# Optimization experiments

Measured on AMD Instinct MI355X. Metric: run time of the kernel, lower is better.

## Reference

```python
import jax, jax.numpy as jnp
from jax import lax
import numpy as np

NF = 64      # feature channels
G = 8        # mask groups
NBR = 3      # top-k neighbors
PATCH = 7    # correlation patch size (patches[0])
CORK = 3     # correlation / unfold kernel size
PAD_COR = 1  # (CORK-1)//2
PAD_S = 4    # PAD_COR + (PATCH-1)//2
ADD = 6      # 2*PAD_S - CORK + 1
B, H, W = 4, 96, 96


def leaky(x):
    return jnp.where(x >= 0, x, 0.1 * x)


def _conv(x, w, b, pad):
    y = lax.conv_general_dilated(x, w, (1, 1), [(pad[0], pad[0]), (pad[1], pad[1])],
                                 dimension_numbers=('NCHW', 'OIHW', 'NCHW'))
    return y + b[None, :, None, None]


def _normalize(x, eps=1e-12):
    n = jnp.sqrt(jnp.sum(x * x, axis=1, keepdims=True))
    return x / jnp.maximum(n, eps)


def _correlation(f1, f2):
    # spatial-correlation-sampler: kernel=3, patch=7, stride=1, pad=1, dilations=1
    # out[b, ph*7+pw, i, j] = sum_{c,u,v} f1p[b,c,i+u,j+v] * f2p[b,c,i+u+ph-3, j+v+pw-3]
    # (unnormalized; only topk indices are consumed downstream, so any positive
    #  constant scale is irrelevant)
    Bx, C, Hx, Wx = f1.shape
    f1p = jnp.pad(f1, ((0, 0), (0, 0), (PAD_COR, PAD_COR), (PAD_COR, PAD_COR)))
    f2p = jnp.pad(f2, ((0, 0), (0, 0), (PAD_S, PAD_S), (PAD_S, PAD_S)))
    outs = []
    for ph in range(PATCH):
        for pw in range(PATCH):
            s = jnp.sum(f1p * f2p[:, :, ph:ph + Hx + 2, pw:pw + Wx + 2], axis=1)  # [B,H+2,W+2]
            o = sum(s[:, u:u + Hx, v:v + Wx] for u in range(CORK) for v in range(CORK))
            outs.append(o)
    return jnp.stack(outs, axis=1)  # [B, 49, H, W]


def setup_inputs() -> dict:
    key = jax.random.key(0)
    ks = jax.random.split(key, 16)

    def wt(k, shape):
        fan_in = shape[1] * shape[2] * shape[3]
        return jax.random.normal(k, shape, jnp.float32) * (1.0 / np.sqrt(fan_in))

    return {
        'ref_fea_l': jax.random.normal(ks[0], (B, NF, H, W), jnp.float32),
        'w1': wt(ks[1], (NF, NF * 2, 3, 3)), 'b1': jnp.zeros((NF,), jnp.float32),
        'w2': wt(ks[2], (NF, NF, 3, 3)),     'b2': jnp.zeros((NF,), jnp.float32),
        'w3': wt(ks[3], (NF, NF, 7, 1)),     'b3': jnp.zeros((NF,), jnp.float32),
        'w4': wt(ks[4], (NF, NF, 1, 7)),     'b4': jnp.zeros((NF,), jnp.float32),
        'wm': wt(ks[5], (G * CORK ** 2, NF, 3, 3)), 'bm': jnp.zeros((G * CORK ** 2,), jnp.float32),
        'wnn': wt(ks[6], (NF, NF * NBR, 3, 3)), 'bnn': jnp.zeros((NF,), jnp.float32),
        'wf': wt(ks[7], (NF, NF * 2, 3, 3)),    'bf': jnp.zeros((NF,), jnp.float32),
    }


def reference(ref_fea_l, w1, b1, w2, b2, w3, b3, w4, b4, wm, bm, wnn, bnn, wf, bf):
    Bx, C, Hx, Wx = ref_fea_l.shape
    nbr_fea = ref_fea_l  # aliased in the original forward

    # mask branch
    x = jnp.concatenate([nbr_fea, ref_fea_l], axis=1)
    x = leaky(_conv(x, w1, b1, (1, 1)))
    x = leaky(_conv(x, w2, b2, (1, 1)))
    x = leaky(_conv(x, w3, b3, (3, 0)))
    x = leaky(_conv(x, w4, b4, (0, 3)))
    mask = _conv(x, wm, bm, (1, 1)).reshape(Bx, G, 1, CORK ** 2, Hx, Wx)

    # correlation + topk neighbor displacements
    nref = _normalize(ref_fea_l)
    corr = _correlation(nref, nref)                     # [B,49,H,W]
    _, idx = lax.top_k(corr.transpose(0, 2, 3, 1), NBR)  # [B,H,W,NBR]

    # flat indices into the (H+6)x(W+6) unfold grid
    ph = idx // PATCH
    pw = idx % PATCH
    yy = jnp.arange(Hx)[:, None, None]
    xx = jnp.arange(Wx)[None, :, None]
    flat = ((ph + yy) * (Wx + ADD) + (pw + xx)).reshape(Bx, Hx * Wx * NBR)

    # unfold (im2col) of nbr features with pad 4, then gather chosen 3x3 patches
    nbr_pad = jnp.pad(nbr_fea, ((0, 0), (0, 0), (PAD_S, PAD_S), (PAD_S, PAD_S)))
    patches = lax.conv_general_dilated_patches(nbr_pad, (CORK, CORK), (1, 1), 'VALID',
                                               dimension_numbers=('NCHW', 'OIHW', 'NCHW'))
    pl = patches.reshape(Bx, C * CORK ** 2, -1).transpose(0, 2, 1)  # [B, (H+6)(W+6), C*9]
    gath = jnp.take_along_axis(pl, flat[:, :, None], axis=1)        # [B, HW*NBR, C*9]
    gath = gath.reshape(Bx * Hx * Wx, NBR * C, CORK, CORK)

    # conv over gathered patches then modulated mask-weighted reduce
    g = leaky(_conv(gath, wnn, bnn, (1, 1)))                         # [BHW, C, 3, 3]
    g = g.reshape(Bx, Hx, Wx, C, CORK ** 2).transpose(0, 3, 4, 1, 2)
    g = g.reshape(Bx, G, C // G, CORK ** 2, Hx, Wx)
    agg = leaky(jnp.sum(g * mask, axis=3).reshape(Bx, C, Hx, Wx))

    out = leaky(_conv(jnp.concatenate([ref_fea_l, agg], axis=1), wf, bf, (1, 1)))
    return out
```

## Files before the change

kernel.cpp:

```cpp
#include <hip/hip_runtime.h>
#include <hip/hip_bf16.h>

constexpr int BATCH = 4;
constexpr int H = 96, W = 96, HW = H * W;
constexpr int NBR = 3;

using bf16x8 = __attribute__((ext_vector_type(8))) short;
using f32x4 = __attribute__((ext_vector_type(4))) float;

static __device__ __forceinline__ float leakyf(float x) {
    return x >= 0.f ? x : 0.1f * x;
}

static __device__ __forceinline__ short f2bf(float x) {
    __hip_bfloat16 h = __float2bfloat16(x);
    return *reinterpret_cast<short*>(&h);
}

static __device__ __forceinline__ float bf2f(short s) {
    __hip_bfloat16 h = *reinterpret_cast<__hip_bfloat16*>(&s);
    return __bfloat162float(h);
}

__global__ __launch_bounds__(256) void k_pre(const float* __restrict__ ref,
                                             short* __restrict__ reft,
                                             float* __restrict__ nrn) {
    int p = blockIdx.x * 256 + threadIdx.x;
    if (p >= BATCH * HW) return;
    int b = p / HW, ij = p % HW;
    const float* src = ref + b * 64 * HW + ij;
    float v[64];
    float ss = 0.f;
#pragma unroll
    for (int c = 0; c < 64; ++c) {
        v[c] = src[c * HW];
        ss += v[c] * v[c];
    }
    float inv = 1.f / fmaxf(sqrtf(ss), 1e-12f);
    short* rd = reft + (size_t)p * 64;
#pragma unroll
    for (int cc = 0; cc < 8; ++cc) {
        bf16x8 o;
#pragma unroll
        for (int j = 0; j < 8; ++j) o[j] = f2bf(v[cc * 8 + j]);
        *(bf16x8*)(rd + cc * 8) = o;
    }
    float* nd = nrn + b * 64 * HW + ij;
#pragma unroll
    for (int c = 0; c < 64; ++c) nd[c * HW] = v[c] * inv;
}

static __device__ __forceinline__ void packw(const float* __restrict__ src,
                                             short* __restrict__ dst, int i,
                                             int OC, int ICt, int ICsrc, int KH,
                                             int KW, int NT, int fold) {
    int e = i & 7, l = (i >> 3) & 63;
    int rest = i >> 9;
    int nt = rest % NT;
    rest /= NT;
    int ICK = ICt >> 5;
    int kk = rest % ICK;
    int tap = rest / ICK;
    int ic = kk * 32 + (l >> 4) * 8 + e;
    int oc = nt * 16 + (l & 15);
    int u = tap / KW, v = tap % KW;
    float val = 0.f;
    if (oc < OC) {
        val = src[((oc * ICsrc + ic) * KH + u) * KW + v];
        if (fold) val += src[((oc * ICsrc + 64 + ic) * KH + u) * KW + v];
    }
    dst[i] = f2bf(val);
}

constexpr int E1 = 36864, E2 = 36864, E3 = 28672, E4 = 28672, E5 = 46080,
              E6 = 73728, E7 = 110592;
constexpr int C1 = E1, C2 = C1 + E2, C3 = C2 + E3, C4 = C3 + E4, C5 = C4 + E5,
              C6 = C5 + E6, C7 = C6 + E7, CT = C7 + 8;
__global__ void k_prep_all(const float* __restrict__ w1,
                           const float* __restrict__ w2,
                           const float* __restrict__ w3,
                           const float* __restrict__ w4,
                           const float* __restrict__ wm,
                           const float* __restrict__ wf,
                           const float* __restrict__ wnn,
                           short* __restrict__ P1, short* __restrict__ P2,
                           short* __restrict__ P3, short* __restrict__ P4,
                           short* __restrict__ PM, short* __restrict__ PF,
                           short* __restrict__ B2, short* __restrict__ zpad) {
    int i = blockIdx.x * 256 + threadIdx.x;
    if (i >= CT) return;
    if (i < C1) {
        packw(w1, P1, i, 64, 64, 128, 3, 3, 4, 1);
    } else if (i < C2) {
        packw(w2, P2, i - C1, 64, 64, 64, 3, 3, 4, 0);
    } else if (i < C3) {
        packw(w3, P3, i - C2, 64, 64, 64, 7, 1, 4, 0);
    } else if (i < C4) {
        packw(w4, P4, i - C3, 64, 64, 64, 1, 7, 4, 0);
    } else if (i < C5) {
        packw(wm, PM, i - C4, 72, 64, 64, 3, 3, 5, 0);
    } else if (i < C6) {
        packw(wf, PF, i - C5, 64, 128, 128, 3, 3, 4, 0);
    } else if (i < C7) {
        int j = i - C6;
        int e = j & 7, l = (j >> 3) & 63;
        int t = (j >> 9) % 9;
        int h2 = (j / (512 * 9)) % 2;
        int n = (j / (512 * 9 * 2)) % 3;
        int nt = j / (512 * 9 * 2 * 3);
        int oc = nt * 16 + (l & 15);
        int c = h2 * 32 + (l >> 4) * 8 + e;
        int u = t / 3, v = t % 3;
        B2[j] = f2bf(wnn[((oc * 192 + n * 64 + c) * 3 + u) * 3 + v]);
    } else {
        zpad[i - C7] = 0;
    }
}

template <int KH, int KW, int IC, int OC, int OMODE, bool BLDS, int NSPL>
__global__ __launch_bounds__(256) void k_cmfma(
    const short* __restrict__ inA, const short* __restrict__ inB,
    const short* __restrict__ Bp, const float* __restrict__ bias,
    void* __restrict__ outp) {
    constexpr int TI = 8, TJ = 16;
    constexpr int PH = (KH - 1) / 2, PW = (KW - 1) / 2;
    constexpr int LR = TI + KH - 1, LC = TJ + KW - 1;
    constexpr int ICB = IC * 2;
    constexpr int LS = (ICB == 128) ? 7 : 8;
    constexpr int ICK = IC / 32;
    constexpr int NTF = (OC + 15) / 16;
    constexpr int NTb = NTF / NSPL;
    constexpr int TAPS = KH * KW;
    constexpr int NOCT = ICB / 16;
    __shared__ char Xs[LR * LC * ICB];
    __shared__ short Bs[BLDS ? TAPS * ICK * NTb * 512 : 8];
    const int tj0 = blockIdx.x * TJ, ti0 = blockIdx.y * TI;
    const int b = blockIdx.z / NSPL;
    const int nt0 = (blockIdx.z % NSPL) * NTb;
    const int tid = threadIdx.x;
    if (BLDS) {
        for (int u2 = tid; u2 < TAPS * ICK * NTb * 64; u2 += 256) {
            int l2 = u2 & 63;
            int rest = u2 >> 6;
            int nt = rest % NTb;
            int qk = rest / NTb;
            ((bf16x8*)Bs)[u2] = ((const bf16x8*)Bp)[(qk * NTF + nt0 + nt) * 64 + l2];
        }
    }
    for (int u2 = tid; u2 < LR * LC * NOCT; u2 += 256) {
        int oct = u2 % NOCT;
        int hp = u2 / NOCT;
        int hr = hp / LC, hc = hp % LC;
        int gi = ti0 + hr - PH, gj = tj0 + hc - PW;
        bf16x8 v = {};
        if (gi >= 0 && gi < H && gj >= 0 && gj < W) {
            const short* s = (oct < 8) ? inA : inB;
            v = *(const bf16x8*)(s + (size_t)(b * HW + gi * W + gj) * 64 +
                                 (oct & 7) * 8);
        }
        int byte = hp * ICB + oct * 16;
        byte ^= ((byte >> LS) & 7) << 4;
        *(bf16x8*)(Xs + byte) = v;
    }
    __syncthreads();
    const int wave = tid >> 6, l = tid & 63;
    const int r = l & 15, q = l >> 4;
    const int mt0 = wave * 2;
    int p0 = mt0 * 16 + r, p1 = p0 + 16;
    int li0 = p0 >> 4, lj0 = p0 & 15, li1 = p1 >> 4, lj1 = p1 & 15;
    f32x4 acc[2][NTb] = {};
#pragma unroll
    for (int t = 0; t < TAPS; ++t) {
        const int u = t / KW, v = t % KW;
        int hp0 = (li0 + u) * LC + (lj0 + v);
        int hp1 = (li1 + u) * LC + (lj1 + v);
#pragma unroll
        for (int kk = 0; kk < ICK; ++kk) {
            int ab0 = hp0 * ICB + kk * 64 + q * 16;
            ab0 ^= ((ab0 >> LS) & 7) << 4;
            int ab1 = hp1 * ICB + kk * 64 + q * 16;
            ab1 ^= ((ab1 >> LS) & 7) << 4;
            bf16x8 a0 = *(const bf16x8*)(Xs + ab0);
            bf16x8 a1 = *(const bf16x8*)(Xs + ab1);
            const short* bbase =
                BLDS ? (const short*)Bs + (t * ICK + kk) * NTb * 512 + l * 8
                     : Bp + ((t * ICK + kk) * NTF + nt0) * 512 + l * 8;
#pragma unroll
            for (int nt = 0; nt < NTb; ++nt) {
                bf16x8 bv = *(const bf16x8*)(bbase + nt * 512);
                acc[0][nt] =
                    __builtin_amdgcn_mfma_f32_16x16x32_bf16(a0, bv, acc[0][nt], 0, 0, 0);
                acc[1][nt] =
                    __builtin_amdgcn_mfma_f32_16x16x32_bf16(a1, bv, acc[1][nt], 0, 0, 0);
            }
        }
    }
    const int col = l & 15;
#pragma unroll
    for (int mt = 0; mt < 2; ++mt)
#pragma unroll
        for (int nt = 0; nt < NTb; ++nt) {
            int oc = (nt0 + nt) * 16 + col;
            float bs = (oc < OC) ? bias[oc] : 0.f;
#pragma unroll
            for (int j = 0; j < 4; ++j) {
                int p = (mt0 + mt) * 16 + q * 4 + j;
                int gi = ti0 + (p >> 4), gj = tj0 + (p & 15);
                float val = acc[mt][nt][j] + bs;
                if (OMODE == 0) {
                    val = leakyf(val);
                    *((short*)outp + (size_t)(b * HW + gi * W + gj) * 64 + oc) =
                        f2bf(val);
                } else if (OMODE == 1) {
                    if (oc < 72)
                        *((short*)outp + (size_t)(b * HW + gi * W + gj) * 72 + oc) =
                            f2bf(val);
                } else {
                    val = leakyf(val);
                    *((float*)outp + (size_t)(b * 64 + oc) * HW + gi * W + gj) = val;
                }
            }
        }
}

__global__ void k_corr2(const float* __restrict__ nr, float* __restrict__ S) {
    int idx = blockIdx.x * 256 + threadIdx.x;
    if (idx >= BATCH * 49 * 98 * 49) return;
    int xp = idx % 49, x0 = xp * 2, x1 = x0 + 1;
    int y = (idx / 49) % 98;
    int d = (idx / (49 * 98)) % 49;
    int b = idx / (49 * 98 * 49);
    int dy = d / 7, dx = d % 7;
    float* row = S + ((size_t)(b * 49 + d)) * (98 * 98) + y * 98;
    if (d > 24) {
        int yy = y + dy - 3;
        if (yy < 0 || yy >= 98) {
            row[x0] = 0.f;
            row[x1] = 0.f;
        } else {
            if (x0 + dx - 3 < 0 || x0 + dx - 3 >= 98) row[x0] = 0.f;
            if (x1 + dx - 3 < 0 || x1 + dx - 3 >= 98) row[x1] = 0.f;
        }
        return;
    }
    int f1i = y - 1, f2i = y + dy - 4;
    float r0 = 0.f, r1 = 0.f;
    if (f1i >= 0 && f1i < H && f2i >= 0 && f2i < H) {
        int f1j0 = x0 - 1, f2j0 = x0 + dx - 4;
        bool v0 = f1j0 >= 0 && f1j0 < W && f2j0 >= 0 && f2j0 < W;
        bool v1 = f1j0 + 1 >= 0 && f1j0 + 1 < W && f2j0 + 1 >= 0 && f2j0 + 1 < W;
        const float* p1 = nr + (size_t)b * 64 * HW + f1i * W + f1j0;
        const float* p2 = nr + (size_t)b * 64 * HW + f2i * W + f2j0;
        if (v0 && v1) {
#pragma unroll 16
            for (int c = 0; c < 64; ++c) {
                float2 a = *(const float2*)(p1 + c * HW);
                float2 q = *(const float2*)(p2 + c * HW);
                r0 = fmaf(a.x, q.x, r0);
                r1 = fmaf(a.y, q.y, r1);
            }
        } else {
            if (v0) {
#pragma unroll 16
                for (int c = 0; c < 64; ++c) r0 = fmaf(p1[c * HW], p2[c * HW], r0);
            }
            if (v1) {
#pragma unroll 16
                for (int c = 0; c < 64; ++c)
                    r1 = fmaf(p1[1 + c * HW], p2[1 + c * HW], r1);
            }
        }
    }
    row[x0] = r0;
    row[x1] = r1;
    if (d < 24) {
        int y2 = y + dy - 3;
        if (y2 >= 0 && y2 < 98) {
            float* mrow = S + ((size_t)(b * 49 + 48 - d)) * (98 * 98) + y2 * 98;
            int x20 = x0 + dx - 3;
            if (x20 >= 0 && x20 < 98) mrow[x20] = r0;
            if (x20 + 1 >= 0 && x20 + 1 < 98) mrow[x20 + 1] = r1;
        }
    }
}

__global__ void k_topk(const float* __restrict__ S, int* __restrict__ idx3) {
    int p = blockIdx.x * 256 + threadIdx.x;
    if (p >= BATCH * HW) return;
    int b = p / HW, i = (p % HW) / W, j = p % W;
    float v0 = -1e30f, v1 = -1e30f, v2 = -1e30f;
    int d0 = 0, d1 = 0, d2 = 0;
    for (int d = 0; d < 49; ++d) {
        const float* s = S + ((b * 49 + d) * 98 + i) * 98 + j;
        float v = 0.f;
#pragma unroll
        for (int u = 0; u < 3; ++u)
#pragma unroll
            for (int vv = 0; vv < 3; ++vv) v += s[u * 98 + vv];
        if (v > v0) {
            v2 = v1; d2 = d1; v1 = v0; d1 = d0; v0 = v; d0 = d;
        } else if (v > v1) {
            v2 = v1; d2 = d1; v1 = v; d1 = d;
        } else if (v > v2) {
            v2 = v; d2 = d;
        }
    }
    idx3[p * 3 + 0] = d0;
    idx3[p * 3 + 1] = d1;
    idx3[p * 3 + 2] = d2;
}

__global__ __launch_bounds__(512, 4) void k_agg_mfma(
    const short* __restrict__ refT, const int* __restrict__ idx3,
    const short* __restrict__ B2, const float* __restrict__ bnn,
    const short* __restrict__ maskT, const short* __restrict__ zpad,
    short* __restrict__ agg) {
    constexpr int PX = 32;
    constexpr int BUFB = 36864;
    __shared__ short A_lds[2 * 2 * 18 * 64 * 8];
    __shared__ short sgi[PX][NBR], sgj[PX][NBR];
    const int bid = blockIdx.x;
    const int swz = (bid & 7) * ((int)gridDim.x >> 3) + (bid >> 3);
    const int p0 = swz * PX;
    const int b = p0 / HW;
    const int i0 = (p0 % HW) / W;
    const int j0 = p0 % W;
    const int tid = threadIdx.x;
    const int wave = tid >> 6;
    const int lane = tid & 63;
    if (tid < PX * NBR) {
        int px = tid / NBR, n = tid % NBR;
        int d = idx3[(p0 + px) * NBR + n];
        sgi[px][n] = (short)(i0 + d / 7 - 4);
        sgj[px][n] = (short)(j0 + px + d % 7 - 4);
    }
    __syncthreads();

    auto STAGE = [&](int n, int buf) {
        for (int r2 = wave; r2 < 36; r2 += 8) {
            int kkl = r2 % 18;
            int ph = r2 / 18;
            int rs = kkl >> 1;
            int oh = kkl & 1;
            int c = lane ^ (((lane >> 4) & 3) | (((buf * 36 + r2) & 1) << 2));
            int oct = oh * 4 + (c >> 4);
            int px = ph * 16 + (c & 15);
            int gi = sgi[px][n] + rs / 3;
            int gj = sgj[px][n] + rs % 3;
            const short* src = (gi >= 0 && gi < H && gj >= 0 && gj < W)
                                   ? refT + (size_t)(b * HW + gi * W + gj) * 64 +
                                         oct * 8
                                   : zpad;
            __builtin_amdgcn_global_load_lds(
                (const __attribute__((address_space(1))) void*)src,
                (__attribute__((address_space(3))) void*)((char*)A_lds +
                                                          buf * BUFB + r2 * 1024),
                16, 0, 0);
        }
    };

    const int w = wave & 3;
    const int half = wave >> 2;
    f32x4 acc[9] = {};
    const short* Bw = B2 + (size_t)w * (3 * 2 * 9 * 512) + lane * 8;

    auto COMPUTE = [&](int n, int buf) {
#pragma unroll
        for (int h2 = 0; h2 < 2; ++h2) {
            const short* bb = Bw + (n * 2 + h2) * 9 * 512;
            bf16x8 bv[9];
#pragma unroll
            for (int t = 0; t < 9; ++t) bv[t] = *(const bf16x8*)(bb + t * 512);
#pragma unroll
            for (int rs = 0; rs < 9; ++rs) {
                int kkl = rs * 2 + h2;
                int ab = buf * BUFB + ((((half * 18 + kkl) << 6) + lane) << 4);
                ab ^= ((ab >> 8) & 7) << 4;
                bf16x8 a = *(const bf16x8*)((char*)A_lds + ab);
#pragma unroll
                for (int t = 0; t < 9; ++t) {
                    const int y = rs / 3 - t / 3 + 1;
                    const int x = rs % 3 - t % 3 + 1;
                    if (y >= 0 && y < 3 && x >= 0 && x < 3)
                        acc[y * 3 + x] = __builtin_amdgcn_mfma_f32_16x16x32_bf16(
                            a, bv[t], acc[y * 3 + x], 0, 0, 0);
                }
            }
        }
    };

    STAGE(0, 0);
    STAGE(1, 1);
    __syncthreads();
    COMPUTE(0, 0);
    __syncthreads();
    STAGE(2, 0);
    COMPUTE(1, 1);
    __syncthreads();
    COMPUTE(2, 0);

    const int oc = w * 16 + (lane & 15);
    const float bn = bnn[oc];
    const int mrow = (lane >> 4) * 4;
#pragma unroll
    for (int j = 0; j < 4; ++j) {
        int px = half * 16 + mrow + j;
        int ij = i0 * W + j0 + px;
        const short* mb = maskT + (size_t)(b * HW + ij) * 72 + (oc >> 3) * 9;
        float sacc = 0.f;
#pragma unroll
        for (int yx = 0; yx < 9; ++yx) {
            float gv = leakyf(acc[yx][j] + bn);
            sacc += gv * bf2f(mb[yx]);
        }
        agg[(size_t)(b * HW + ij) * 64 + oc] = f2bf(leakyf(sacc));
    }
}

extern "C" void kernel_launch(void* const* d_in, const int* in_sizes, int n_in,
                              void* d_out, int out_size, void* d_ws,
                              size_t ws_size, hipStream_t stream) {
    const float* ref = (const float*)d_in[0];
    const float* w1 = (const float*)d_in[1];
    const float* b1 = (const float*)d_in[2];
    const float* w2 = (const float*)d_in[3];
    const float* b2 = (const float*)d_in[4];
    const float* w3 = (const float*)d_in[5];
    const float* b3 = (const float*)d_in[6];
    const float* w4 = (const float*)d_in[7];
    const float* b4 = (const float*)d_in[8];
    const float* wm = (const float*)d_in[9];
    const float* bm = (const float*)d_in[10];
    const float* wnn = (const float*)d_in[11];
    const float* bnn = (const float*)d_in[12];
    const float* wf = (const float*)d_in[13];
    const float* bf = (const float*)d_in[14];

    char* ws = (char*)d_ws;
    constexpr size_t O_NRN = 0;
    constexpr size_t O_S = O_NRN + (size_t)BATCH * HW * 64 * 4;
    constexpr size_t O_REFT = O_S + (size_t)BATCH * 49 * 98 * 98 * 4;
    constexpr size_t O_X1 = O_REFT + (size_t)BATCH * HW * 64 * 2;
    constexpr size_t O_X2 = O_X1 + (size_t)BATCH * HW * 64 * 2;
    constexpr size_t O_MASKT = O_X2 + (size_t)BATCH * HW * 64 * 2;
    constexpr size_t O_IDX = O_MASKT + (size_t)BATCH * HW * 72 * 2;
    constexpr size_t O_P1 = O_IDX + (size_t)BATCH * HW * 3 * 4;
    constexpr size_t O_P2 = O_P1 + (size_t)E1 * 2;
    constexpr size_t O_P3 = O_P2 + (size_t)E2 * 2;
    constexpr size_t O_P4 = O_P3 + (size_t)E3 * 2;
    constexpr size_t O_PM = O_P4 + (size_t)E4 * 2;
    constexpr size_t O_PF = O_PM + (size_t)E5 * 2;
    constexpr size_t O_B2 = O_PF + (size_t)E6 * 2;
    constexpr size_t O_ZP = O_B2 + (size_t)E7 * 2;

    float* NRN = (float*)(ws + O_NRN);
    float* S = (float*)(ws + O_S);
    short* REFT = (short*)(ws + O_REFT);
    short* X1 = (short*)(ws + O_X1);
    short* X2 = (short*)(ws + O_X2);
    short* MASKT = (short*)(ws + O_MASKT);
    int* IDX = (int*)(ws + O_IDX);
    short* P1 = (short*)(ws + O_P1);
    short* P2 = (short*)(ws + O_P2);
    short* P3 = (short*)(ws + O_P3);
    short* P4 = (short*)(ws + O_P4);
    short* PM = (short*)(ws + O_PM);
    short* PF = (short*)(ws + O_PF);
    short* B2 = (short*)(ws + O_B2);
    short* ZPAD = (short*)(ws + O_ZP);

    k_pre<<<(BATCH * HW + 255) / 256, 256, 0, stream>>>(ref, REFT, NRN);
    k_prep_all<<<(CT + 255) / 256, 256, 0, stream>>>(w1, w2, w3, w4, wm, wf, wnn,
                                                     P1, P2, P3, P4, PM, PF, B2,
                                                     ZPAD);

    dim3 cgrid4(6, 12, BATCH * 4);
    dim3 cgridm(6, 12, BATCH * 5);
    dim3 cgridf(6, 12, BATCH * 2);
    k_cmfma<3, 3, 64, 64, 0, true, 4><<<cgrid4, 256, 0, stream>>>(REFT, nullptr, P1, b1, X1);
    k_cmfma<3, 3, 64, 64, 0, true, 4><<<cgrid4, 256, 0, stream>>>(X1, nullptr, P2, b2, X2);
    k_cmfma<7, 1, 64, 64, 0, true, 4><<<cgrid4, 256, 0, stream>>>(X2, nullptr, P3, b3, X1);
    k_cmfma<1, 7, 64, 64, 0, true, 4><<<cgrid4, 256, 0, stream>>>(X1, nullptr, P4, b4, X2);
    k_cmfma<3, 3, 64, 72, 1, true, 5><<<cgridm, 256, 0, stream>>>(X2, nullptr, PM, bm, MASKT);

    k_corr2<<<(BATCH * 49 * 98 * 49 + 255) / 256, 256, 0, stream>>>(NRN, S);
    k_topk<<<BATCH * HW / 256, 256, 0, stream>>>(S, IDX);

    k_agg_mfma<<<BATCH * HW / 32, 512, 0, stream>>>(REFT, IDX, B2, bnn, MASKT,
                                                    ZPAD, X1);

    k_cmfma<3, 3, 128, 64, 2, false, 2><<<cgridf, 256, 0, stream>>>(REFT, X1, PF, bf, d_out);
}
```

Baseline: 204.3 us.

## Widen conv output-channel tiles, swizzle block order, pad mask layout for vector loads

Conv blocks now compute two 16-channel output tiles each, with fewer channel splits per block, so each input halo tile staged in LDS is reused across more output channels. The mask conv is padded to 96 channels in three splits, and its output is stored in a 128-wide per-pixel layout with 16-element groups so the aggregation kernel can read eight mask values in one vector load. Block IDs are swizzled across the grid to change scheduling and cache locality. The cost is fewer blocks per launch, more accumulator registers per thread, and a larger mask buffer.

```diff
diff --git a/kernel.cpp b/kernel.cpp
--- a/kernel.cpp
+++ b/kernel.cpp
@@ -72,7 +72,7 @@
     dst[i] = f2bf(val);
 }
 
-constexpr int E1 = 36864, E2 = 36864, E3 = 28672, E4 = 28672, E5 = 46080,
+constexpr int E1 = 36864, E2 = 36864, E3 = 28672, E4 = 28672, E5 = 55296,
               E6 = 73728, E7 = 110592;
 constexpr int C1 = E1, C2 = C1 + E2, C3 = C2 + E3, C4 = C3 + E4, C5 = C4 + E5,
               C6 = C5 + E6, C7 = C6 + E7, CT = C7 + 8;
@@ -98,7 +98,7 @@
     } else if (i < C4) {
         packw(w4, P4, i - C3, 64, 64, 64, 1, 7, 4, 0);
     } else if (i < C5) {
-        packw(wm, PM, i - C4, 72, 64, 64, 3, 3, 5, 0);
+        packw(wm, PM, i - C4, 72, 64, 64, 3, 3, 6, 0);
     } else if (i < C6) {
         packw(wf, PF, i - C5, 64, 128, 128, 3, 3, 4, 0);
     } else if (i < C7) {
@@ -117,7 +117,7 @@
     }
 }
 
-template <int KH, int KW, int IC, int OC, int OMODE, bool BLDS, int NSPL>
+template <int KH, int KW, int IC, int OC, int OMODE, bool BLDS, int NTb, int NSPL>
 __global__ __launch_bounds__(256) void k_cmfma(
     const short* __restrict__ inA, const short* __restrict__ inB,
     const short* __restrict__ Bp, const float* __restrict__ bias,
@@ -128,15 +128,19 @@
     constexpr int ICB = IC * 2;
     constexpr int LS = (ICB == 128) ? 7 : 8;
     constexpr int ICK = IC / 32;
-    constexpr int NTF = (OC + 15) / 16;
-    constexpr int NTb = NTF / NSPL;
+    constexpr int NTF = NTb * NSPL;
     constexpr int TAPS = KH * KW;
     constexpr int NOCT = ICB / 16;
     __shared__ char Xs[LR * LC * ICB];
     __shared__ short Bs[BLDS ? TAPS * ICK * NTb * 512 : 8];
-    const int tj0 = blockIdx.x * TJ, ti0 = blockIdx.y * TI;
-    const int b = blockIdx.z / NSPL;
-    const int nt0 = (blockIdx.z % NSPL) * NTb;
+    const int nb = 72 * (int)gridDim.z;
+    int lid = blockIdx.x + 6 * (blockIdx.y + 12 * blockIdx.z);
+    int swz = (lid & 7) * (nb >> 3) + (lid >> 3);
+    const int zz = swz / 72;
+    const int rem = swz % 72;
+    const int tj0 = (rem % 6) * TJ, ti0 = (rem / 6) * TI;
+    const int b = zz / NSPL;
+    const int nt0 = (zz % NSPL) * NTb;
     const int tid = threadIdx.x;
     if (BLDS) {
         for (int u2 = tid; u2 < TAPS * ICK * NTb * 64; u2 += 256) {
@@ -213,8 +217,8 @@
                         f2bf(val);
                 } else if (OMODE == 1) {
                     if (oc < 72)
-                        *((short*)outp + (size_t)(b * HW + gi * W + gj) * 72 + oc) =
-                            f2bf(val);
+                        *((short*)outp + (size_t)(b * HW + gi * W + gj) * 128 +
+                          (oc / 9) * 16 + (oc % 9)) = f2bf(val);
                 } else {
                     val = leakyf(val);
                     *((float*)outp + (size_t)(b * 64 + oc) * HW + gi * W + gj) = val;
@@ -406,13 +410,16 @@
     for (int j = 0; j < 4; ++j) {
         int px = half * 16 + mrow + j;
         int ij = i0 * W + j0 + px;
-        const short* mb = maskT + (size_t)(b * HW + ij) * 72 + (oc >> 3) * 9;
+        const short* mb = maskT + (size_t)(b * HW + ij) * 128 + (oc >> 3) * 16;
+        bf16x8 m8 = *(const bf16x8*)mb;
+        short m9 = mb[8];
         float sacc = 0.f;
 #pragma unroll
-        for (int yx = 0; yx < 9; ++yx) {
+        for (int yx = 0; yx < 8; ++yx) {
             float gv = leakyf(acc[yx][j] + bn);
-            sacc += gv * bf2f(mb[yx]);
-        }
+            sacc += gv * bf2f(m8[yx]);
+        }
+        sacc += leakyf(acc[8][j] + bn) * bf2f(m9);
         agg[(size_t)(b * HW + ij) * 64 + oc] = f2bf(leakyf(sacc));
     }
 }
@@ -443,7 +450,7 @@
     constexpr size_t O_X1 = O_REFT + (size_t)BATCH * HW * 64 * 2;
     constexpr size_t O_X2 = O_X1 + (size_t)BATCH * HW * 64 * 2;
     constexpr size_t O_MASKT = O_X2 + (size_t)BATCH * HW * 64 * 2;
-    constexpr size_t O_IDX = O_MASKT + (size_t)BATCH * HW * 72 * 2;
+    constexpr size_t O_IDX = O_MASKT + (size_t)BATCH * HW * 128 * 2;
     constexpr size_t O_P1 = O_IDX + (size_t)BATCH * HW * 3 * 4;
     constexpr size_t O_P2 = O_P1 + (size_t)E1 * 2;
     constexpr size_t O_P3 = O_P2 + (size_t)E2 * 2;
@@ -474,14 +481,13 @@
                                                      P1, P2, P3, P4, PM, PF, B2,
                                                      ZPAD);
 
-    dim3 cgrid4(6, 12, BATCH * 4);
-    dim3 cgridm(6, 12, BATCH * 5);
-    dim3 cgridf(6, 12, BATCH * 2);
-    k_cmfma<3, 3, 64, 64, 0, true, 4><<<cgrid4, 256, 0, stream>>>(REFT, nullptr, P1, b1, X1);
-    k_cmfma<3, 3, 64, 64, 0, true, 4><<<cgrid4, 256, 0, stream>>>(X1, nullptr, P2, b2, X2);
-    k_cmfma<7, 1, 64, 64, 0, true, 4><<<cgrid4, 256, 0, stream>>>(X2, nullptr, P3, b3, X1);
-    k_cmfma<1, 7, 64, 64, 0, true, 4><<<cgrid4, 256, 0, stream>>>(X1, nullptr, P4, b4, X2);
-    k_cmfma<3, 3, 64, 72, 1, true, 5><<<cgridm, 256, 0, stream>>>(X2, nullptr, PM, bm, MASKT);
+    dim3 cgrid2(6, 12, BATCH * 2);
+    dim3 cgridm(6, 12, BATCH * 3);
+    k_cmfma<3, 3, 64, 64, 0, true, 2, 2><<<cgrid2, 256, 0, stream>>>(REFT, nullptr, P1, b1, X1);
+    k_cmfma<3, 3, 64, 64, 0, true, 2, 2><<<cgrid2, 256, 0, stream>>>(X1, nullptr, P2, b2, X2);
+    k_cmfma<7, 1, 64, 64, 0, true, 2, 2><<<cgrid2, 256, 0, stream>>>(X2, nullptr, P3, b3, X1);
+    k_cmfma<1, 7, 64, 64, 0, true, 2, 2><<<cgrid2, 256, 0, stream>>>(X1, nullptr, P4, b4, X2);
+    k_cmfma<3, 3, 64, 72, 1, true, 2, 3><<<cgridm, 256, 0, stream>>>(X2, nullptr, PM, bm, MASKT);
 
     k_corr2<<<(BATCH * 49 * 98 * 49 + 255) / 256, 256, 0, stream>>>(NRN, S);
     k_topk<<<BATCH * HW / 256, 256, 0, stream>>>(S, IDX);
@@ -489,5 +495,5 @@
     k_agg_mfma<<<BATCH * HW / 32, 512, 0, stream>>>(REFT, IDX, B2, bnn, MASKT,
                                                     ZPAD, X1);
 
-    k_cmfma<3, 3, 128, 64, 2, false, 2><<<cgridf, 256, 0, stream>>>(REFT, X1, PF, bf, d_out);
-}
+    k_cmfma<3, 3, 128, 64, 2, false, 2, 2><<<cgrid2, 256, 0, stream>>>(REFT, X1, PF, bf, d_out);
+}
```

After: 213.1 us. 4.3% more time.

## Double pixel tile per block in aggregation MFMA kernel to reuse weight fragments

Applied to the files above, without the earlier changes.

The gather-conv-aggregate kernel now processes 64 pixels per block instead of 32. Each wave keeps two accumulator sets and issues two MFMAs per loaded weight fragment, halving B-fragment global loads per pixel. Pixel row/column is computed per pixel because a 64-pixel tile can cross a row boundary. LDS use doubles to 144 KB (double buffered), and register pressure rises, so launch bounds drop to 2 blocks per CU and the grid halves, reducing occupancy.

```diff
diff --git a/kernel.cpp b/kernel.cpp
--- a/kernel.cpp
+++ b/kernel.cpp
@@ -310,39 +310,39 @@
     idx3[p * 3 + 2] = d2;
 }
 
-__global__ __launch_bounds__(512, 4) void k_agg_mfma(
+__global__ __launch_bounds__(512, 2) void k_agg_mfma(
     const short* __restrict__ refT, const int* __restrict__ idx3,
     const short* __restrict__ B2, const float* __restrict__ bnn,
     const short* __restrict__ maskT, const short* __restrict__ zpad,
     short* __restrict__ agg) {
-    constexpr int PX = 32;
-    constexpr int BUFB = 36864;
-    __shared__ short A_lds[2 * 2 * 18 * 64 * 8];
+    constexpr int PX = 64;
+    constexpr int BUFB = 73728;
+    __shared__ short A_lds[2 * 4 * 18 * 64 * 8];
     __shared__ short sgi[PX][NBR], sgj[PX][NBR];
     const int bid = blockIdx.x;
     const int swz = (bid & 7) * ((int)gridDim.x >> 3) + (bid >> 3);
     const int p0 = swz * PX;
     const int b = p0 / HW;
-    const int i0 = (p0 % HW) / W;
-    const int j0 = p0 % W;
     const int tid = threadIdx.x;
     const int wave = tid >> 6;
     const int lane = tid & 63;
     if (tid < PX * NBR) {
         int px = tid / NBR, n = tid % NBR;
-        int d = idx3[(p0 + px) * NBR + n];
-        sgi[px][n] = (short)(i0 + d / 7 - 4);
-        sgj[px][n] = (short)(j0 + px + d % 7 - 4);
+        int pix = p0 + px;
+        int ipx = (pix % HW) / W, jpx = pix % W;
+        int d = idx3[pix * NBR + n];
+        sgi[px][n] = (short)(ipx + d / 7 - 4);
+        sgj[px][n] = (short)(jpx + d % 7 - 4);
     }
     __syncthreads();
 
     auto STAGE = [&](int n, int buf) {
-        for (int r2 = wave; r2 < 36; r2 += 8) {
+        for (int r2 = wave; r2 < 72; r2 += 8) {
             int kkl = r2 % 18;
             int ph = r2 / 18;
             int rs = kkl >> 1;
             int oh = kkl & 1;
-            int c = lane ^ (((lane >> 4) & 3) | (((buf * 36 + r2) & 1) << 2));
+            int c = lane ^ (((lane >> 4) & 3) | ((r2 & 1) << 2));
             int oct = oh * 4 + (c >> 4);
             int px = ph * 16 + (c & 15);
             int gi = sgi[px][n] + rs / 3;
@@ -360,8 +360,8 @@
     };
 
     const int w = wave & 3;
-    const int half = wave >> 2;
-    f32x4 acc[9] = {};
+    const int hgrp = wave >> 2;
+    f32x4 acc[2][9] = {};
     const short* Bw = B2 + (size_t)w * (3 * 2 * 9 * 512) + lane * 8;
 
     auto COMPUTE = [&](int n, int buf) {
@@ -374,16 +374,27 @@
 #pragma unroll
             for (int rs = 0; rs < 9; ++rs) {
                 int kkl = rs * 2 + h2;
-                int ab = buf * BUFB + ((((half * 18 + kkl) << 6) + lane) << 4);
-                ab ^= ((ab >> 8) & 7) << 4;
-                bf16x8 a = *(const bf16x8*)((char*)A_lds + ab);
+                bf16x8 a0, a1;
+                {
+                    int ab = buf * BUFB +
+                             (((((hgrp * 2) * 18 + kkl) << 6) + lane) << 4);
+                    ab ^= ((ab >> 8) & 7) << 4;
+                    a0 = *(const bf16x8*)((char*)A_lds + ab);
+                    int ab1 = buf * BUFB +
+                              (((((hgrp * 2 + 1) * 18 + kkl) << 6) + lane) << 4);
+                    ab1 ^= ((ab1 >> 8) & 7) << 4;
+                    a1 = *(const bf16x8*)((char*)A_lds + ab1);
+                }
 #pragma unroll
                 for (int t = 0; t < 9; ++t) {
                     const int y = rs / 3 - t / 3 + 1;
                     const int x = rs % 3 - t % 3 + 1;
-                    if (y >= 0 && y < 3 && x >= 0 && x < 3)
-                        acc[y * 3 + x] = __builtin_amdgcn_mfma_f32_16x16x32_bf16(
-                            a, bv[t], acc[y * 3 + x], 0, 0, 0);
+                    if (y >= 0 && y < 3 && x >= 0 && x < 3) {
+                        acc[0][y * 3 + x] = __builtin_amdgcn_mfma_f32_16x16x32_bf16(
+                            a0, bv[t], acc[0][y * 3 + x], 0, 0, 0);
+                        acc[1][y * 3 + x] = __builtin_amdgcn_mfma_f32_16x16x32_bf16(
+                            a1, bv[t], acc[1][y * 3 + x], 0, 0, 0);
+                    }
                 }
             }
         }
@@ -403,17 +414,20 @@
     const float bn = bnn[oc];
     const int mrow = (lane >> 4) * 4;
 #pragma unroll
-    for (int j = 0; j < 4; ++j) {
-        int px = half * 16 + mrow + j;
-        int ij = i0 * W + j0 + px;
-        const short* mb = maskT + (size_t)(b * HW + ij) * 72 + (oc >> 3) * 9;
-        float sacc = 0.f;
-#pragma unroll
-        for (int yx = 0; yx < 9; ++yx) {
-            float gv = leakyf(acc[yx][j] + bn);
-            sacc += gv * bf2f(mb[yx]);
-        }
-        agg[(size_t)(b * HW + ij) * 64 + oc] = f2bf(leakyf(sacc));
+    for (int pp = 0; pp < 2; ++pp) {
+#pragma unroll
+        for (int j = 0; j < 4; ++j) {
+            int px = (hgrp * 2 + pp) * 16 + mrow + j;
+            int ij = p0 + px;
+            const short* mb = maskT + (size_t)ij * 72 + (oc >> 3) * 9;
+            float sacc = 0.f;
+#pragma unroll
+            for (int yx = 0; yx < 9; ++yx) {
+                float gv = leakyf(acc[pp][yx][j] + bn);
+                sacc += gv * bf2f(mb[yx]);
+            }
+            agg[(size_t)ij * 64 + oc] = f2bf(leakyf(sacc));
+        }
     }
 }
 
@@ -486,7 +500,7 @@
     k_corr2<<<(BATCH * 49 * 98 * 49 + 255) / 256, 256, 0, stream>>>(NRN, S);
     k_topk<<<BATCH * HW / 256, 256, 0, stream>>>(S, IDX);
 
-    k_agg_mfma<<<BATCH * HW / 32, 512, 0, stream>>>(REFT, IDX, B2, bnn, MASKT,
+    k_agg_mfma<<<BATCH * HW / 64, 512, 0, stream>>>(REFT, IDX, B2, bnn, MASKT,
                                                     ZPAD, X1);
 
     k_cmfma<3, 3, 128, 64, 2, false, 2><<<cgridf, 256, 0, stream>>>(REFT, X1, PF, bf, d_out);
```

Measured after the change: 217.6 us. 6.5% more time.

## Fuse correlation and top-k work into conv launches as extra tail blocks

Applied to the files above, without the earlier changes.

Correlation and top-k become device functions run by extra blocks appended to the grids of the first two conv kernels. The grid is flattened to 1D with the tile index decoded from blockIdx.x. The independent correlation chain then overlaps with the conv chain and two kernel launches go away. The cost is that tail blocks share LDS allocation and launch bounds with the conv blocks, which may reduce occupancy for the correlation work.

```diff
diff --git a/kernel.cpp b/kernel.cpp
--- a/kernel.cpp
+++ b/kernel.cpp
@@ -117,114 +117,9 @@
     }
 }
 
-template <int KH, int KW, int IC, int OC, int OMODE, bool BLDS, int NSPL>
-__global__ __launch_bounds__(256) void k_cmfma(
-    const short* __restrict__ inA, const short* __restrict__ inB,
-    const short* __restrict__ Bp, const float* __restrict__ bias,
-    void* __restrict__ outp) {
-    constexpr int TI = 8, TJ = 16;
-    constexpr int PH = (KH - 1) / 2, PW = (KW - 1) / 2;
-    constexpr int LR = TI + KH - 1, LC = TJ + KW - 1;
-    constexpr int ICB = IC * 2;
-    constexpr int LS = (ICB == 128) ? 7 : 8;
-    constexpr int ICK = IC / 32;
-    constexpr int NTF = (OC + 15) / 16;
-    constexpr int NTb = NTF / NSPL;
-    constexpr int TAPS = KH * KW;
-    constexpr int NOCT = ICB / 16;
-    __shared__ char Xs[LR * LC * ICB];
-    __shared__ short Bs[BLDS ? TAPS * ICK * NTb * 512 : 8];
-    const int tj0 = blockIdx.x * TJ, ti0 = blockIdx.y * TI;
-    const int b = blockIdx.z / NSPL;
-    const int nt0 = (blockIdx.z % NSPL) * NTb;
-    const int tid = threadIdx.x;
-    if (BLDS) {
-        for (int u2 = tid; u2 < TAPS * ICK * NTb * 64; u2 += 256) {
-            int l2 = u2 & 63;
-            int rest = u2 >> 6;
-            int nt = rest % NTb;
-            int qk = rest / NTb;
-            ((bf16x8*)Bs)[u2] = ((const bf16x8*)Bp)[(qk * NTF + nt0 + nt) * 64 + l2];
-        }
-    }
-    for (int u2 = tid; u2 < LR * LC * NOCT; u2 += 256) {
-        int oct = u2 % NOCT;
-        int hp = u2 / NOCT;
-        int hr = hp / LC, hc = hp % LC;
-        int gi = ti0 + hr - PH, gj = tj0 + hc - PW;
-        bf16x8 v = {};
-        if (gi >= 0 && gi < H && gj >= 0 && gj < W) {
-            const short* s = (oct < 8) ? inA : inB;
-            v = *(const bf16x8*)(s + (size_t)(b * HW + gi * W + gj) * 64 +
-                                 (oct & 7) * 8);
-        }
-        int byte = hp * ICB + oct * 16;
-        byte ^= ((byte >> LS) & 7) << 4;
-        *(bf16x8*)(Xs + byte) = v;
-    }
-    __syncthreads();
-    const int wave = tid >> 6, l = tid & 63;
-    const int r = l & 15, q = l >> 4;
-    const int mt0 = wave * 2;
-    int p0 = mt0 * 16 + r, p1 = p0 + 16;
-    int li0 = p0 >> 4, lj0 = p0 & 15, li1 = p1 >> 4, lj1 = p1 & 15;
-    f32x4 acc[2][NTb] = {};
-#pragma unroll
-    for (int t = 0; t < TAPS; ++t) {
-        const int u = t / KW, v = t % KW;
-        int hp0 = (li0 + u) * LC + (lj0 + v);
-        int hp1 = (li1 + u) * LC + (lj1 + v);
-#pragma unroll
-        for (int kk = 0; kk < ICK; ++kk) {
-            int ab0 = hp0 * ICB + kk * 64 + q * 16;
-            ab0 ^= ((ab0 >> LS) & 7) << 4;
-            int ab1 = hp1 * ICB + kk * 64 + q * 16;
-            ab1 ^= ((ab1 >> LS) & 7) << 4;
-            bf16x8 a0 = *(const bf16x8*)(Xs + ab0);
-            bf16x8 a1 = *(const bf16x8*)(Xs + ab1);
-            const short* bbase =
-                BLDS ? (const short*)Bs + (t * ICK + kk) * NTb * 512 + l * 8
-                     : Bp + ((t * ICK + kk) * NTF + nt0) * 512 + l * 8;
-#pragma unroll
-            for (int nt = 0; nt < NTb; ++nt) {
-                bf16x8 bv = *(const bf16x8*)(bbase + nt * 512);
-                acc[0][nt] =
-                    __builtin_amdgcn_mfma_f32_16x16x32_bf16(a0, bv, acc[0][nt], 0, 0, 0);
-                acc[1][nt] =
-                    __builtin_amdgcn_mfma_f32_16x16x32_bf16(a1, bv, acc[1][nt], 0, 0, 0);
-            }
-        }
-    }
-    const int col = l & 15;
-#pragma unroll
-    for (int mt = 0; mt < 2; ++mt)
-#pragma unroll
-        for (int nt = 0; nt < NTb; ++nt) {
-            int oc = (nt0 + nt) * 16 + col;
-            float bs = (oc < OC) ? bias[oc] : 0.f;
-#pragma unroll
-            for (int j = 0; j < 4; ++j) {
-                int p = (mt0 + mt) * 16 + q * 4 + j;
-                int gi = ti0 + (p >> 4), gj = tj0 + (p & 15);
-                float val = acc[mt][nt][j] + bs;
-                if (OMODE == 0) {
-                    val = leakyf(val);
-                    *((short*)outp + (size_t)(b * HW + gi * W + gj) * 64 + oc) =
-                        f2bf(val);
-                } else if (OMODE == 1) {
-                    if (oc < 72)
-                        *((short*)outp + (size_t)(b * HW + gi * W + gj) * 72 + oc) =
-                            f2bf(val);
-                } else {
-                    val = leakyf(val);
-                    *((float*)outp + (size_t)(b * 64 + oc) * HW + gi * W + gj) = val;
-                }
-            }
-        }
-}
-
-__global__ void k_corr2(const float* __restrict__ nr, float* __restrict__ S) {
-    int idx = blockIdx.x * 256 + threadIdx.x;
+static __device__ void corr2_body(const float* __restrict__ nr,
+                                  float* __restrict__ S, int blk) {
+    int idx = blk * 256 + threadIdx.x;
     if (idx >= BATCH * 49 * 98 * 49) return;
     int xp = idx % 49, x0 = xp * 2, x1 = x0 + 1;
     int y = (idx / 49) % 98;
@@ -284,8 +179,9 @@
     }
 }
 
-__global__ void k_topk(const float* __restrict__ S, int* __restrict__ idx3) {
-    int p = blockIdx.x * 256 + threadIdx.x;
+static __device__ void topk_body(const float* __restrict__ S,
+                                 int* __restrict__ idx3, int blk) {
+    int p = blk * 256 + threadIdx.x;
     if (p >= BATCH * HW) return;
     int b = p / HW, i = (p % HW) / W, j = p % W;
     float v0 = -1e30f, v1 = -1e30f, v2 = -1e30f;
@@ -308,6 +204,123 @@
     idx3[p * 3 + 0] = d0;
     idx3[p * 3 + 1] = d1;
     idx3[p * 3 + 2] = d2;
+}
+
+template <int KH, int KW, int IC, int OC, int OMODE, bool BLDS, int NSPL, int TAIL>
+__global__ __launch_bounds__(256) void k_cmfma(
+    const short* __restrict__ inA, const short* __restrict__ inB,
+    const short* __restrict__ Bp, const float* __restrict__ bias,
+    void* __restrict__ outp, const float* __restrict__ taux,
+    float* __restrict__ tS, int* __restrict__ tidx, int convblks) {
+    if (TAIL != 0 && (int)blockIdx.x >= convblks) {
+        int xb = (int)blockIdx.x - convblks;
+        if (TAIL == 1)
+            corr2_body(taux, tS, xb);
+        else
+            topk_body(taux, tidx, xb);
+        return;
+    }
+    constexpr int TI = 8, TJ = 16;
+    constexpr int PH = (KH - 1) / 2, PW = (KW - 1) / 2;
+    constexpr int LR = TI + KH - 1, LC = TJ + KW - 1;
+    constexpr int ICB = IC * 2;
+    constexpr int LS = (ICB == 128) ? 7 : 8;
+    constexpr int ICK = IC / 32;
+    constexpr int NTF = (OC + 15) / 16;
+    constexpr int NTb = NTF / NSPL;
+    constexpr int TAPS = KH * KW;
+    constexpr int NOCT = ICB / 16;
+    __shared__ char Xs[LR * LC * ICB];
+    __shared__ short Bs[BLDS ? TAPS * ICK * NTb * 512 : 8];
+    const int lid = blockIdx.x;
+    const int tj0 = (lid % 6) * TJ, ti0 = ((lid / 6) % 12) * TI;
+    const int zz = lid / 72;
+    const int b = zz / NSPL;
+    const int nt0 = (zz % NSPL) * NTb;
+    const int tid = threadIdx.x;
+    if (BLDS) {
+        for (int u2 = tid; u2 < TAPS * ICK * NTb * 64; u2 += 256) {
+            int l2 = u2 & 63;
+            int rest = u2 >> 6;
+            int nt = rest % NTb;
+            int qk = rest / NTb;
+            ((bf16x8*)Bs)[u2] = ((const bf16x8*)Bp)[(qk * NTF + nt0 + nt) * 64 + l2];
+        }
+    }
+    for (int u2 = tid; u2 < LR * LC * NOCT; u2 += 256) {
+        int oct = u2 % NOCT;
+        int hp = u2 / NOCT;
+        int hr = hp / LC, hc = hp % LC;
+        int gi = ti0 + hr - PH, gj = tj0 + hc - PW;
+        bf16x8 v = {};
+        if (gi >= 0 && gi < H && gj >= 0 && gj < W) {
+            const short* s = (oct < 8) ? inA : inB;
+            v = *(const bf16x8*)(s + (size_t)(b * HW + gi * W + gj) * 64 +
+                                 (oct & 7) * 8);
+        }
+        int byte = hp * ICB + oct * 16;
+        byte ^= ((byte >> LS) & 7) << 4;
+        *(bf16x8*)(Xs + byte) = v;
+    }
+    __syncthreads();
+    const int wave = tid >> 6, l = tid & 63;
+    const int r = l & 15, q = l >> 4;
+    const int mt0 = wave * 2;
+    int p0 = mt0 * 16 + r, p1 = p0 + 16;
+    int li0 = p0 >> 4, lj0 = p0 & 15, li1 = p1 >> 4, lj1 = p1 & 15;
+    f32x4 acc[2][NTb] = {};
+#pragma unroll
+    for (int t = 0; t < TAPS; ++t) {
+        const int u = t / KW, v = t % KW;
+        int hp0 = (li0 + u) * LC + (lj0 + v);
+        int hp1 = (li1 + u) * LC + (lj1 + v);
+#pragma unroll
+        for (int kk = 0; kk < ICK; ++kk) {
+            int ab0 = hp0 * ICB + kk * 64 + q * 16;
+            ab0 ^= ((ab0 >> LS) & 7) << 4;
+            int ab1 = hp1 * ICB + kk * 64 + q * 16;
+            ab1 ^= ((ab1 >> LS) & 7) << 4;
+            bf16x8 a0 = *(const bf16x8*)(Xs + ab0);
+            bf16x8 a1 = *(const bf16x8*)(Xs + ab1);
+            const short* bbase =
+                BLDS ? (const short*)Bs + (t * ICK + kk) * NTb * 512 + l * 8
+                     : Bp + ((t * ICK + kk) * NTF + nt0) * 512 + l * 8;
+#pragma unroll
+            for (int nt = 0; nt < NTb; ++nt) {
+                bf16x8 bv = *(const bf16x8*)(bbase + nt * 512);
+                acc[0][nt] =
+                    __builtin_amdgcn_mfma_f32_16x16x32_bf16(a0, bv, acc[0][nt], 0, 0, 0);
+                acc[1][nt] =
+                    __builtin_amdgcn_mfma_f32_16x16x32_bf16(a1, bv, acc[1][nt], 0, 0, 0);
+            }
+        }
+    }
+    const int col = l & 15;
+#pragma unroll
+    for (int mt = 0; mt < 2; ++mt)
+#pragma unroll
+        for (int nt = 0; nt < NTb; ++nt) {
+            int oc = (nt0 + nt) * 16 + col;
+            float bs = (oc < OC) ? bias[oc] : 0.f;
+#pragma unroll
+            for (int j = 0; j < 4; ++j) {
+                int p = (mt0 + mt) * 16 + q * 4 + j;
+                int gi = ti0 + (p >> 4), gj = tj0 + (p & 15);
+                float val = acc[mt][nt][j] + bs;
+                if (OMODE == 0) {
+                    val = leakyf(val);
+                    *((short*)outp + (size_t)(b * HW + gi * W + gj) * 64 + oc) =
+                        f2bf(val);
+                } else if (OMODE == 1) {
+                    if (oc < 72)
+                        *((short*)outp + (size_t)(b * HW + gi * W + gj) * 72 + oc) =
+                            f2bf(val);
+                } else {
+                    val = leakyf(val);
+                    *((float*)outp + (size_t)(b * 64 + oc) * HW + gi * W + gj) = val;
+                }
+            }
+        }
 }
 
 __global__ __launch_bounds__(512, 4) void k_agg_mfma(
@@ -469,25 +482,29 @@
     short* B2 = (short*)(ws + O_B2);
     short* ZPAD = (short*)(ws + O_ZP);
 
+    constexpr int CONVB = 6 * 12 * BATCH * 4;
+    constexpr int CORRB = (BATCH * 49 * 98 * 49 + 255) / 256;
+    constexpr int TOPKB = BATCH * HW / 256;
+
     k_pre<<<(BATCH * HW + 255) / 256, 256, 0, stream>>>(ref, REFT, NRN);
     k_prep_all<<<(CT + 255) / 256, 256, 0, stream>>>(w1, w2, w3, w4, wm, wf, wnn,
                                                      P1, P2, P3, P4, PM, PF, B2,
                                                      ZPAD);
 
-    dim3 cgrid4(6, 12, BATCH * 4);
-    dim3 cgridm(6, 12, BATCH * 5);
-    dim3 cgridf(6, 12, BATCH * 2);
-    k_cmfma<3, 3, 64, 64, 0, true, 4><<<cgrid4, 256, 0, stream>>>(REFT, nullptr, P1, b1, X1);
-    k_cmfma<3, 3, 64, 64, 0, true, 4><<<cgrid4, 256, 0, stream>>>(X1, nullptr, P2, b2, X2);
-    k_cmfma<7, 1, 64, 64, 0, true, 4><<<cgrid4, 256, 0, stream>>>(X2, nullptr, P3, b3, X1);
-    k_cmfma<1, 7, 64, 64, 0, true, 4><<<cgrid4, 256, 0, stream>>>(X1, nullptr, P4, b4, X2);
-    k_cmfma<3, 3, 64, 72, 1, true, 5><<<cgridm, 256, 0, stream>>>(X2, nullptr, PM, bm, MASKT);
-
-    k_corr2<<<(BATCH * 49 * 98 * 49 + 255) / 256, 256, 0, stream>>>(NRN, S);
-    k_topk<<<BATCH * HW / 256, 256, 0, stream>>>(S, IDX);
+    k_cmfma<3, 3, 64, 64, 0, true, 4, 1><<<CONVB + CORRB, 256, 0, stream>>>(
+        REFT, nullptr, P1, b1, X1, NRN, S, nullptr, CONVB);
+    k_cmfma<3, 3, 64, 64, 0, true, 4, 2><<<CONVB + TOPKB, 256, 0, stream>>>(
+        X1, nullptr, P2, b2, X2, S, nullptr, IDX, CONVB);
+    k_cmfma<7, 1, 64, 64, 0, true, 4, 0><<<CONVB, 256, 0, stream>>>(
+        X2, nullptr, P3, b3, X1, nullptr, nullptr, nullptr, CONVB);
+    k_cmfma<1, 7, 64, 64, 0, true, 4, 0><<<CONVB, 256, 0, stream>>>(
+        X1, nullptr, P4, b4, X2, nullptr, nullptr, nullptr, CONVB);
+    k_cmfma<3, 3, 64, 72, 1, true, 5, 0><<<6 * 12 * BATCH * 5, 256, 0, stream>>>(
+        X2, nullptr, PM, bm, MASKT, nullptr, nullptr, nullptr, 6 * 12 * BATCH * 5);
 
     k_agg_mfma<<<BATCH * HW / 32, 512, 0, stream>>>(REFT, IDX, B2, bnn, MASKT,
                                                     ZPAD, X1);
 
-    k_cmfma<3, 3, 128, 64, 2, false, 2><<<cgridf, 256, 0, stream>>>(REFT, X1, PF, bf, d_out);
-}
+    k_cmfma<3, 3, 128, 64, 2, false, 2, 0><<<6 * 12 * BATCH * 2, 256, 0, stream>>>(
+        REFT, X1, PF, bf, d_out, nullptr, nullptr, nullptr, 6 * 12 * BATCH * 2);
+}
```

Result: no change. 203.6 us (-0.4%).
